# Kernel tuning notes

Hardware: AMD Instinct MI355X
Metric: run time of the kernel (lower is better)

The kernel has to match this reference:

```python
import jax, jax.numpy as jnp
import numpy as np

NEG = -9e15  # mask value from original (-9000000000000000.0)

def setup_inputs() -> dict:
    key = jax.random.key(0)
    k1, k2, k3, k4 = jax.random.split(key, 4)
    N, nin, nout = 8192, 256, 128
    h = jax.random.normal(k1, (N, nin), dtype=jnp.float32)
    adj = jax.random.randint(k2, (N, N), 0, 2, dtype=jnp.int32)
    w = jax.random.normal(k3, (nin, nout), dtype=jnp.float32)
    v = jax.random.normal(k4, (2 * nout, 1), dtype=jnp.float32)
    return {"h": h, "adj": adj, "w": w, "v": v}

def reference(h, adj, w, v):
    nout = w.shape[1]
    hw = h @ w                      # [N, nout]
    hw1 = hw @ v[:nout]             # [N, 1]
    hw2 = hw @ v[nout:]             # [N, 1]
    eij = hw1 + hw2.T               # [N, N] additive outer-sum scores
    att = jnp.where(adj > 0, eij, jnp.float32(NEG))
    att = jax.nn.softmax(att, axis=1)
    return att @ hw                 # [N, nout]
```

## Files before the change

kernel.cpp:

```cpp
#include <hip/hip_runtime.h>
#include <math.h>

#define N_ROWS 8192
#define NIN    256
#define NOUT   128
#define CUTOFF 45.0f
#define TOPK   32
#define NBINS  256
#define RANGE  384.0f
#define MAXL   256

__device__ __forceinline__ float block_max_256(float v, float* red) {
#pragma unroll
    for (int off = 32; off > 0; off >>= 1)
        v = fmaxf(v, __shfl_down(v, off, 64));
    if ((threadIdx.x & 63) == 0) red[threadIdx.x >> 6] = v;
    __syncthreads();
    float r = fmaxf(fmaxf(red[0], red[1]), fmaxf(red[2], red[3]));
    __syncthreads();
    return r;
}

__global__ __launch_bounds__(256) void k_sw(const float* __restrict__ h,
                                            const float* __restrict__ w,
                                            const float* __restrict__ v,
                                            float* __restrict__ s) {
    __shared__ float wv[NIN];
    int tid = threadIdx.x;
    const float* wr = w + (size_t)tid * NOUT;
    const float* v2 = v + NOUT;
    float acc = 0.f;
#pragma unroll
    for (int n = 0; n < NOUT; n += 4) {
        float4 a = *(const float4*)(wr + n);
        float4 b = *(const float4*)(v2 + n);
        acc = fmaf(a.x, b.x, acc);
        acc = fmaf(a.y, b.y, acc);
        acc = fmaf(a.z, b.z, acc);
        acc = fmaf(a.w, b.w, acc);
    }
    wv[tid] = acc;
    __syncthreads();

    int wid  = tid >> 6;
    int lane = tid & 63;
    float4 wv4 = *(const float4*)(wv + lane * 4);
    int row0 = blockIdx.x * 8 + wid * 2;
#pragma unroll
    for (int r = 0; r < 2; ++r) {
        const float* hr = h + (size_t)(row0 + r) * NIN;
        float4 hv = *(const float4*)(hr + lane * 4);
        float a = hv.x * wv4.x;
        a = fmaf(hv.y, wv4.y, a);
        a = fmaf(hv.z, wv4.z, a);
        a = fmaf(hv.w, wv4.w, a);
#pragma unroll
        for (int off = 32; off > 0; off >>= 1)
            a += __shfl_down(a, off, 64);
        if (lane == 0) s[row0 + r] = a;
    }
}

__global__ __launch_bounds__(256) void k_top(const float* __restrict__ s_g,
                                             int* __restrict__ L,
                                             float* __restrict__ Ls,
                                             int* __restrict__ nL_p,
                                             float* __restrict__ T_p) {
    __shared__ float sd[N_ROWS];
    __shared__ float red[4];
    __shared__ int   hist[NBINS];
    __shared__ int   c;
    __shared__ float Tsh;
    int tid = threadIdx.x;
    hist[tid] = 0;
    float mloc = -INFINITY;
    for (int j = tid; j < N_ROWS; j += 256) {
        float v = s_g[j];
        sd[j] = v;
        mloc = fmaxf(mloc, v);
    }
    __syncthreads();
    float mstar = block_max_256(mloc, red);
    const float invw = (float)NBINS / RANGE;
    for (int j = tid; j < N_ROWS; j += 256) {
        int b = (int)((mstar - sd[j]) * invw);
        b = b < 0 ? 0 : (b > NBINS - 1 ? NBINS - 1 : b);
        atomicAdd(&hist[b], 1);
    }
    __syncthreads();
    if (tid == 0) {
        int cum = 0, B = NBINS - 1;
        for (int b = 0; b < NBINS; ++b) {
            cum += hist[b];
            if (cum >= TOPK) { B = b; break; }
        }
        Tsh = mstar - (float)(B + 1) * (RANGE / (float)NBINS) - CUTOFF;
        *T_p = Tsh;
        c = 0;
    }
    __syncthreads();
    float T = Tsh;
    for (int j = tid; j < N_ROWS; j += 256) {
        float v = sd[j];
        if (v >= T) {
            int p = atomicAdd(&c, 1);
            L[p]  = j;
            Ls[p] = v;
        }
    }
    __syncthreads();
    if (tid == 0) *nL_p = c;
}

__global__ __launch_bounds__(128) void k_hwL(const float* __restrict__ h,
                                             const float* __restrict__ w,
                                             const int* __restrict__ L,
                                             const int* __restrict__ nL_p,
                                             float* __restrict__ hwL2) {
    int nL = *nL_p;
    if (nL > MAXL) return;
    int nLp = (nL + 7) & ~7;
    int k = threadIdx.x;
    int sidx = ((k & 63) << 1) | (k >> 6);
    for (int t = blockIdx.x; t < nLp; t += gridDim.x) {
        float acc = 0.f;
        if (t < nL) {
            const float* hr = h + (size_t)L[t] * NIN;
#pragma unroll 4
            for (int n = 0; n < NIN; n += 4) {
                float4 hv = *(const float4*)(hr + n);
                acc = fmaf(hv.x, w[(size_t)(n + 0) * NOUT + k], acc);
                acc = fmaf(hv.y, w[(size_t)(n + 1) * NOUT + k], acc);
                acc = fmaf(hv.z, w[(size_t)(n + 2) * NOUT + k], acc);
                acc = fmaf(hv.w, w[(size_t)(n + 3) * NOUT + k], acc);
            }
        }
        hwL2[(size_t)t * NOUT + sidx] = acc;
    }
}

__global__ __launch_bounds__(256) void k_att4(const int* __restrict__ adj,
                                              const float* __restrict__ s_g,
                                              const float* __restrict__ h,
                                              const float* __restrict__ w,
                                              const float* __restrict__ hwL2,
                                              const int* __restrict__ L,
                                              const float* __restrict__ Ls,
                                              const int* __restrict__ nL_p,
                                              const float* __restrict__ T_p,
                                              float* __restrict__ out) {
    __shared__ float pwsh[4][MAXL];
    int wid  = threadIdx.x >> 6;
    int lane = threadIdx.x & 63;
    int i    = blockIdx.x * 4 + wid;
    int   nL = nL_p[0];
    float T  = T_p[0];
    const int* arow = adj + (size_t)i * N_ROWS;

    bool fast = (nL <= MAXL);
    float sv[4] = {-INFINITY, -INFINITY, -INFINITY, -INFINITY};
    float m = -INFINITY;

    if (fast) {
#pragma unroll
        for (int p = 0; p < 4; ++p) {
            int t = p * 64 + lane;
            if (t < nL) {
                int j = L[t];
                sv[p] = (arow[j] > 0) ? Ls[t] : -INFINITY;
            }
        }
        float mm = fmaxf(fmaxf(sv[0], sv[1]), fmaxf(sv[2], sv[3]));
#pragma unroll
        for (int off = 32; off > 0; off >>= 1)
            mm = fmaxf(mm, __shfl_down(mm, off, 64));
        m = __shfl(mm, 0, 64);
    }

    if (fast && (m - CUTOFF >= T)) {
#pragma unroll
        for (int p = 0; p < 4; ++p)
            pwsh[wid][p * 64 + lane] = __expf(sv[p] - m);
        int nLp = (nL + 7) & ~7;
        const float* pwr = pwsh[wid];
        float acc0 = 0.f, acc1 = 0.f, den = 0.f;
        for (int t = 0; t < nLp; t += 4) {
            float4 pw = *(const float4*)(pwr + t);
            const float* g = hwL2 + (size_t)t * NOUT + (lane << 1);
            float2 g0 = *(const float2*)(g);
            float2 g1 = *(const float2*)(g + NOUT);
            float2 g2 = *(const float2*)(g + 2 * NOUT);
            float2 g3 = *(const float2*)(g + 3 * NOUT);
            den += (pw.x + pw.y) + (pw.z + pw.w);
            acc0 = fmaf(pw.x, g0.x, acc0); acc1 = fmaf(pw.x, g0.y, acc1);
            acc0 = fmaf(pw.y, g1.x, acc0); acc1 = fmaf(pw.y, g1.y, acc1);
            acc0 = fmaf(pw.z, g2.x, acc0); acc1 = fmaf(pw.z, g2.y, acc1);
            acc0 = fmaf(pw.w, g3.x, acc0); acc1 = fmaf(pw.w, g3.y, acc1);
        }
        out[(size_t)i * NOUT + lane]      = acc0 / den;
        out[(size_t)i * NOUT + 64 + lane] = acc1 / den;
        return;
    }

    float m2 = -INFINITY;
    for (int j0 = lane * 4; j0 < N_ROWS; j0 += 256) {
        int4   a  = *(const int4*)(arow + j0);
        float4 sx = *(const float4*)(s_g + j0);
        if (a.x > 0) m2 = fmaxf(m2, sx.x);
        if (a.y > 0) m2 = fmaxf(m2, sx.y);
        if (a.z > 0) m2 = fmaxf(m2, sx.z);
        if (a.w > 0) m2 = fmaxf(m2, sx.w);
    }
#pragma unroll
    for (int off = 32; off > 0; off >>= 1)
        m2 = fmaxf(m2, __shfl_down(m2, off, 64));
    m2 = __shfl(m2, 0, 64);

    if (m2 > -INFINITY) {
        float acc0 = 0.f, acc1 = 0.f, den = 0.f;
        for (int j = 0; j < N_ROWS; ++j) {
            if (arow[j] > 0) {
                float p = __expf(s_g[j] - m2);
                if (p > 0.f) {
                    den += p;
                    const float* hr = h + (size_t)j * NIN;
                    float d0 = 0.f, d1 = 0.f;
                    for (int nn = 0; nn < NIN; ++nn) {
                        float hv = hr[nn];
                        d0 = fmaf(hv, w[(size_t)nn * NOUT + lane], d0);
                        d1 = fmaf(hv, w[(size_t)nn * NOUT + 64 + lane], d1);
                    }
                    acc0 = fmaf(p, d0, acc0);
                    acc1 = fmaf(p, d1, acc1);
                }
            }
        }
        out[(size_t)i * NOUT + lane]      = acc0 / den;
        out[(size_t)i * NOUT + 64 + lane] = acc1 / den;
    } else {
        float cs[4] = {0.f, 0.f, 0.f, 0.f};
        for (int r = 0; r < N_ROWS; ++r) {
            const float* hr = h + (size_t)r * NIN;
#pragma unroll
            for (int q = 0; q < 4; ++q)
                cs[q] += hr[lane + q * 64];
        }
        float acc0 = 0.f, acc1 = 0.f;
        for (int nn = 0; nn < NIN; ++nn) {
            float csv = __shfl(cs[nn >> 6], nn & 63, 64);
            acc0 = fmaf(csv, w[(size_t)nn * NOUT + lane], acc0);
            acc1 = fmaf(csv, w[(size_t)nn * NOUT + 64 + lane], acc1);
        }
        out[(size_t)i * NOUT + lane]      = acc0 / (float)N_ROWS;
        out[(size_t)i * NOUT + 64 + lane] = acc1 / (float)N_ROWS;
    }
}

extern "C" void kernel_launch(void* const* d_in, const int* in_sizes, int n_in,
                              void* d_out, int out_size, void* d_ws, size_t ws_size,
                              hipStream_t stream) {
    const float* h   = (const float*)d_in[0];
    const int*   adj = (const int*)  d_in[1];
    const float* w   = (const float*)d_in[2];
    const float* v   = (const float*)d_in[3];
    float* out = (float*)d_out;

    char* ws = (char*)d_ws;
    float* hwL = (float*)(ws);
    size_t o   = (size_t)MAXL * NOUT * 4;
    float* s   = (float*)(ws + o);  o += (size_t)N_ROWS * 4;
    int*   L   = (int*)  (ws + o);  o += (size_t)N_ROWS * 4;
    float* Ls  = (float*)(ws + o);  o += (size_t)N_ROWS * 4;
    int*   nL  = (int*)  (ws + o);  o += 16;
    float* T   = (float*)(ws + o);

    k_sw  <<<N_ROWS / 8, 256, 0, stream>>>(h, w, v, s);
    k_top <<<1,          256, 0, stream>>>(s, L, Ls, nL, T);
    k_hwL <<<128,        128, 0, stream>>>(h, w, L, nL, hwL);
    k_att4<<<N_ROWS / 4, 256, 0, stream>>>(adj, s, h, w, hwL, L, Ls, nL, T, out);
}
```

Before: 392.2 us.

## Process four attention rows per wavefront to reuse hwL loads

The attention kernel now has each wavefront handle four output rows instead of one. The gathered candidate indices and scores are loaded once for all four rows, and each hwL2 tile read from memory feeds four accumulators. This cuts global and L2 traffic on the projected-feature table and the index loads, at the cost of more registers, more shared memory, and a grid a quarter the size. Rows that fail the cutoff check still drop to the exact slow path one at a time, and the denominator is now computed separately through a wave reduction.

```diff
diff --git a/kernel.cpp b/kernel.cpp
--- a/kernel.cpp
+++ b/kernel.cpp
@@ -139,7 +139,7 @@
     }
 }
 
-__global__ __launch_bounds__(256) void k_att4(const int* __restrict__ adj,
+__global__ __launch_bounds__(256) void k_att5(const int* __restrict__ adj,
                                               const float* __restrict__ s_g,
                                               const float* __restrict__ h,
                                               const float* __restrict__ w,
@@ -149,110 +149,149 @@
                                               const int* __restrict__ nL_p,
                                               const float* __restrict__ T_p,
                                               float* __restrict__ out) {
-    __shared__ float pwsh[4][MAXL];
+    __shared__ __align__(16) float pwsh[4][4][MAXL];
     int wid  = threadIdx.x >> 6;
     int lane = threadIdx.x & 63;
-    int i    = blockIdx.x * 4 + wid;
+    int i0   = blockIdx.x * 16 + wid * 4;
     int   nL = nL_p[0];
     float T  = T_p[0];
-    const int* arow = adj + (size_t)i * N_ROWS;
-
-    bool fast = (nL <= MAXL);
-    float sv[4] = {-INFINITY, -INFINITY, -INFINITY, -INFINITY};
-    float m = -INFINITY;
-
-    if (fast) {
+    bool fastAll = (nL <= MAXL);
+    bool cert[4] = {false, false, false, false};
+    float den[4] = {1.f, 1.f, 1.f, 1.f};
+
+    if (fastAll) {
+        int   lt[4];
+        float ls[4];
 #pragma unroll
         for (int p = 0; p < 4; ++p) {
             int t = p * 64 + lane;
-            if (t < nL) {
-                int j = L[t];
-                sv[p] = (arow[j] > 0) ? Ls[t] : -INFINITY;
-            }
-        }
-        float mm = fmaxf(fmaxf(sv[0], sv[1]), fmaxf(sv[2], sv[3]));
-#pragma unroll
-        for (int off = 32; off > 0; off >>= 1)
-            mm = fmaxf(mm, __shfl_down(mm, off, 64));
-        m = __shfl(mm, 0, 64);
-    }
-
-    if (fast && (m - CUTOFF >= T)) {
-#pragma unroll
-        for (int p = 0; p < 4; ++p)
-            pwsh[wid][p * 64 + lane] = __expf(sv[p] - m);
+            lt[p] = (t < nL) ? L[t]  : -1;
+            ls[p] = (t < nL) ? Ls[t] : 0.f;
+        }
+        float sv[4][4];
+#pragma unroll
+        for (int r = 0; r < 4; ++r) {
+            const int* arow = adj + (size_t)(i0 + r) * N_ROWS;
+#pragma unroll
+            for (int p = 0; p < 4; ++p)
+                sv[r][p] = (lt[p] >= 0 && arow[lt[p]] > 0) ? ls[p] : -INFINITY;
+        }
+#pragma unroll
+        for (int r = 0; r < 4; ++r) {
+            float mm = fmaxf(fmaxf(sv[r][0], sv[r][1]), fmaxf(sv[r][2], sv[r][3]));
+#pragma unroll
+            for (int off = 32; off > 0; off >>= 1)
+                mm = fmaxf(mm, __shfl_down(mm, off, 64));
+            float m = __shfl(mm, 0, 64);
+            cert[r] = (m - CUTOFF >= T);
+            float dp = 0.f;
+#pragma unroll
+            for (int p = 0; p < 4; ++p) {
+                float pw = __expf(sv[r][p] - m);
+                pwsh[wid][r][p * 64 + lane] = pw;
+                dp += pw;
+            }
+#pragma unroll
+            for (int off = 32; off > 0; off >>= 1)
+                dp += __shfl_down(dp, off, 64);
+            den[r] = __shfl(dp, 0, 64);
+        }
         int nLp = (nL + 7) & ~7;
-        const float* pwr = pwsh[wid];
-        float acc0 = 0.f, acc1 = 0.f, den = 0.f;
+        float a0[4] = {0.f, 0.f, 0.f, 0.f};
+        float a1[4] = {0.f, 0.f, 0.f, 0.f};
         for (int t = 0; t < nLp; t += 4) {
-            float4 pw = *(const float4*)(pwr + t);
+            float4 p0 = *(const float4*)&pwsh[wid][0][t];
+            float4 p1 = *(const float4*)&pwsh[wid][1][t];
+            float4 p2 = *(const float4*)&pwsh[wid][2][t];
+            float4 p3 = *(const float4*)&pwsh[wid][3][t];
             const float* g = hwL2 + (size_t)t * NOUT + (lane << 1);
             float2 g0 = *(const float2*)(g);
             float2 g1 = *(const float2*)(g + NOUT);
             float2 g2 = *(const float2*)(g + 2 * NOUT);
             float2 g3 = *(const float2*)(g + 3 * NOUT);
-            den += (pw.x + pw.y) + (pw.z + pw.w);
-            acc0 = fmaf(pw.x, g0.x, acc0); acc1 = fmaf(pw.x, g0.y, acc1);
-            acc0 = fmaf(pw.y, g1.x, acc0); acc1 = fmaf(pw.y, g1.y, acc1);
-            acc0 = fmaf(pw.z, g2.x, acc0); acc1 = fmaf(pw.z, g2.y, acc1);
-            acc0 = fmaf(pw.w, g3.x, acc0); acc1 = fmaf(pw.w, g3.y, acc1);
-        }
-        out[(size_t)i * NOUT + lane]      = acc0 / den;
-        out[(size_t)i * NOUT + 64 + lane] = acc1 / den;
-        return;
-    }
-
-    float m2 = -INFINITY;
-    for (int j0 = lane * 4; j0 < N_ROWS; j0 += 256) {
-        int4   a  = *(const int4*)(arow + j0);
-        float4 sx = *(const float4*)(s_g + j0);
-        if (a.x > 0) m2 = fmaxf(m2, sx.x);
-        if (a.y > 0) m2 = fmaxf(m2, sx.y);
-        if (a.z > 0) m2 = fmaxf(m2, sx.z);
-        if (a.w > 0) m2 = fmaxf(m2, sx.w);
-    }
-#pragma unroll
-    for (int off = 32; off > 0; off >>= 1)
-        m2 = fmaxf(m2, __shfl_down(m2, off, 64));
-    m2 = __shfl(m2, 0, 64);
-
-    if (m2 > -INFINITY) {
-        float acc0 = 0.f, acc1 = 0.f, den = 0.f;
-        for (int j = 0; j < N_ROWS; ++j) {
-            if (arow[j] > 0) {
-                float p = __expf(s_g[j] - m2);
-                if (p > 0.f) {
-                    den += p;
-                    const float* hr = h + (size_t)j * NIN;
-                    float d0 = 0.f, d1 = 0.f;
-                    for (int nn = 0; nn < NIN; ++nn) {
-                        float hv = hr[nn];
-                        d0 = fmaf(hv, w[(size_t)nn * NOUT + lane], d0);
-                        d1 = fmaf(hv, w[(size_t)nn * NOUT + 64 + lane], d1);
+            a0[0] = fmaf(p0.x, g0.x, a0[0]); a1[0] = fmaf(p0.x, g0.y, a1[0]);
+            a0[0] = fmaf(p0.y, g1.x, a0[0]); a1[0] = fmaf(p0.y, g1.y, a1[0]);
+            a0[0] = fmaf(p0.z, g2.x, a0[0]); a1[0] = fmaf(p0.z, g2.y, a1[0]);
+            a0[0] = fmaf(p0.w, g3.x, a0[0]); a1[0] = fmaf(p0.w, g3.y, a1[0]);
+            a0[1] = fmaf(p1.x, g0.x, a0[1]); a1[1] = fmaf(p1.x, g0.y, a1[1]);
+            a0[1] = fmaf(p1.y, g1.x, a0[1]); a1[1] = fmaf(p1.y, g1.y, a1[1]);
+            a0[1] = fmaf(p1.z, g2.x, a0[1]); a1[1] = fmaf(p1.z, g2.y, a1[1]);
+            a0[1] = fmaf(p1.w, g3.x, a0[1]); a1[1] = fmaf(p1.w, g3.y, a1[1]);
+            a0[2] = fmaf(p2.x, g0.x, a0[2]); a1[2] = fmaf(p2.x, g0.y, a1[2]);
+            a0[2] = fmaf(p2.y, g1.x, a0[2]); a1[2] = fmaf(p2.y, g1.y, a1[2]);
+            a0[2] = fmaf(p2.z, g2.x, a0[2]); a1[2] = fmaf(p2.z, g2.y, a1[2]);
+            a0[2] = fmaf(p2.w, g3.x, a0[2]); a1[2] = fmaf(p2.w, g3.y, a1[2]);
+            a0[3] = fmaf(p3.x, g0.x, a0[3]); a1[3] = fmaf(p3.x, g0.y, a1[3]);
+            a0[3] = fmaf(p3.y, g1.x, a0[3]); a1[3] = fmaf(p3.y, g1.y, a1[3]);
+            a0[3] = fmaf(p3.z, g2.x, a0[3]); a1[3] = fmaf(p3.z, g2.y, a1[3]);
+            a0[3] = fmaf(p3.w, g3.x, a0[3]); a1[3] = fmaf(p3.w, g3.y, a1[3]);
+        }
+#pragma unroll
+        for (int r = 0; r < 4; ++r) {
+            if (cert[r]) {
+                out[(size_t)(i0 + r) * NOUT + lane]      = a0[r] / den[r];
+                out[(size_t)(i0 + r) * NOUT + 64 + lane] = a1[r] / den[r];
+            }
+        }
+        if (cert[0] && cert[1] && cert[2] && cert[3]) return;
+    }
+
+    for (int r = 0; r < 4; ++r) {
+        if (cert[r]) continue;
+        int i = i0 + r;
+        const int* arow = adj + (size_t)i * N_ROWS;
+        float m2 = -INFINITY;
+        for (int j0 = lane * 4; j0 < N_ROWS; j0 += 256) {
+            int4   a  = *(const int4*)(arow + j0);
+            float4 sx = *(const float4*)(s_g + j0);
+            if (a.x > 0) m2 = fmaxf(m2, sx.x);
+            if (a.y > 0) m2 = fmaxf(m2, sx.y);
+            if (a.z > 0) m2 = fmaxf(m2, sx.z);
+            if (a.w > 0) m2 = fmaxf(m2, sx.w);
+        }
+#pragma unroll
+        for (int off = 32; off > 0; off >>= 1)
+            m2 = fmaxf(m2, __shfl_down(m2, off, 64));
+        m2 = __shfl(m2, 0, 64);
+
+        if (m2 > -INFINITY) {
+            float acc0 = 0.f, acc1 = 0.f, dn = 0.f;
+            for (int j = 0; j < N_ROWS; ++j) {
+                if (arow[j] > 0) {
+                    float p = __expf(s_g[j] - m2);
+                    if (p > 0.f) {
+                        dn += p;
+                        const float* hr = h + (size_t)j * NIN;
+                        float d0 = 0.f, d1 = 0.f;
+                        for (int nn = 0; nn < NIN; ++nn) {
+                            float hv = hr[nn];
+                            d0 = fmaf(hv, w[(size_t)nn * NOUT + lane], d0);
+                            d1 = fmaf(hv, w[(size_t)nn * NOUT + 64 + lane], d1);
+                        }
+                        acc0 = fmaf(p, d0, acc0);
+                        acc1 = fmaf(p, d1, acc1);
                     }
-                    acc0 = fmaf(p, d0, acc0);
-                    acc1 = fmaf(p, d1, acc1);
                 }
             }
-        }
-        out[(size_t)i * NOUT + lane]      = acc0 / den;
-        out[(size_t)i * NOUT + 64 + lane] = acc1 / den;
-    } else {
-        float cs[4] = {0.f, 0.f, 0.f, 0.f};
-        for (int r = 0; r < N_ROWS; ++r) {
-            const float* hr = h + (size_t)r * NIN;
-#pragma unroll
-            for (int q = 0; q < 4; ++q)
-                cs[q] += hr[lane + q * 64];
-        }
-        float acc0 = 0.f, acc1 = 0.f;
-        for (int nn = 0; nn < NIN; ++nn) {
-            float csv = __shfl(cs[nn >> 6], nn & 63, 64);
-            acc0 = fmaf(csv, w[(size_t)nn * NOUT + lane], acc0);
-            acc1 = fmaf(csv, w[(size_t)nn * NOUT + 64 + lane], acc1);
-        }
-        out[(size_t)i * NOUT + lane]      = acc0 / (float)N_ROWS;
-        out[(size_t)i * NOUT + 64 + lane] = acc1 / (float)N_ROWS;
+            out[(size_t)i * NOUT + lane]      = acc0 / dn;
+            out[(size_t)i * NOUT + 64 + lane] = acc1 / dn;
+        } else {
+            float cs[4] = {0.f, 0.f, 0.f, 0.f};
+            for (int rr = 0; rr < N_ROWS; ++rr) {
+                const float* hr = h + (size_t)rr * NIN;
+#pragma unroll
+                for (int q = 0; q < 4; ++q)
+                    cs[q] += hr[lane + q * 64];
+            }
+            float acc0 = 0.f, acc1 = 0.f;
+            for (int nn = 0; nn < NIN; ++nn) {
+                float csv = __shfl(cs[nn >> 6], nn & 63, 64);
+                acc0 = fmaf(csv, w[(size_t)nn * NOUT + lane], acc0);
+                acc1 = fmaf(csv, w[(size_t)nn * NOUT + 64 + lane], acc1);
+            }
+            out[(size_t)i * NOUT + lane]      = acc0 / (float)N_ROWS;
+            out[(size_t)i * NOUT + 64 + lane] = acc1 / (float)N_ROWS;
+        }
     }
 }
 
@@ -274,8 +313,8 @@
     int*   nL  = (int*)  (ws + o);  o += 16;
     float* T   = (float*)(ws + o);
 
-    k_sw  <<<N_ROWS / 8, 256, 0, stream>>>(h, w, v, s);
-    k_top <<<1,          256, 0, stream>>>(s, L, Ls, nL, T);
-    k_hwL <<<128,        128, 0, stream>>>(h, w, L, nL, hwL);
-    k_att4<<<N_ROWS / 4, 256, 0, stream>>>(adj, s, h, w, hwL, L, Ls, nL, T, out);
-}
+    k_sw  <<<N_ROWS / 8,  256, 0, stream>>>(h, w, v, s);
+    k_top <<<1,           256, 0, stream>>>(s, L, Ls, nL, T);
+    k_hwL <<<128,         128, 0, stream>>>(h, w, L, nL, hwL);
+    k_att5<<<N_ROWS / 16, 256, 0, stream>>>(adj, s, h, w, hwL, L, Ls, nL, T, out);
+}
```

Result: no change. 385.7 us (-1.7%).
